# Optimization experiments

Measured on AMD Instinct MI355X. Metric: run time of the kernel, lower is better.

## Reference

```python
import jax, jax.numpy as jnp
import numpy as np


def _topk_corr(h_s, h_t, k):
    """DGMC top-k correspondence: similarity matmul -> top-k -> gather -> dot -> softmax.

    h_s: [B, Ns, C], h_t: [B, Nt, C].
    Mirrors __top_k__ (S_ij = x_s @ x_t^T; topk indices) followed by the
    torch.gather of top-k target embeddings and S_hat = (h_s * h_t[idx]).sum(-1).
    """
    S = jnp.einsum('bsc,btc->bst', h_s, h_t)            # [B, Ns, Nt]
    _, idx = jax.lax.top_k(S, k)                         # [B, Ns, k] (largest sims)
    gathered = jax.vmap(lambda ht, ix: ht[ix])(h_t, idx)  # [B, Ns, k, C]
    S_hat = jnp.einsum('bsc,bskc->bsk', h_s, gathered)    # [B, Ns, k]
    S0 = jax.nn.softmax(S_hat, axis=-1)                   # softmax over k candidates
    return S0, idx


def setup_inputs() -> dict:
    key = jax.random.key(0)
    ks = jax.random.split(key, 4)
    B, Ns, Nt, C = 1, 10000, 10000, 256
    return {
        'eh_s': jax.random.normal(ks[0], (B, Ns, C), jnp.float32),
        'eh_t': jax.random.normal(ks[1], (B, Nt, C), jnp.float32),
        'rh_s': jax.random.normal(ks[2], (B, Ns, C), jnp.float32),
        'rh_t': jax.random.normal(ks[3], (B, Nt, C), jnp.float32),
        'k': 10,
    }


def reference(eh_s, eh_t, rh_s, rh_t, k):
    eS0, eidx = _topk_corr(eh_s, eh_t, k)
    rS0, ridx = _topk_corr(rh_s, rh_t, k)
    # to_sparse via the (all-true, single-graph) dense-batch mask: [B,Ns,k] -> [B*Ns,k]
    B, Ns, kk = eS0.shape
    return eS0.reshape(B * Ns, kk), rS0.reshape(B * Ns, kk), eidx, ridx
```

## Files before the change

kernel.cpp:

```cpp
#include <hip/hip_runtime.h>


typedef __attribute__((ext_vector_type(8)))  short bf16x8;
typedef __attribute__((ext_vector_type(16))) float f32x16;
typedef __attribute__((ext_vector_type(8)))  unsigned short u16x8;

#define K_TOP 10
#define CAND_M 12
#define CDIM 256

#define GLD_LDS(src, dst) \
    __builtin_amdgcn_global_load_lds((const __attribute__((address_space(1))) void*)(src), \
                                     (__attribute__((address_space(3))) void*)(dst), 16, 0, 0)

__device__ __forceinline__ unsigned short f2bf(float f) {
    unsigned u = __float_as_uint(f);
    u += 0x7fffu + ((u >> 16) & 1u);
    return (unsigned short)(u >> 16);
}

__device__ __forceinline__ unsigned umax2(unsigned a, unsigned b) { return a > b ? a : b; }
__device__ __forceinline__ unsigned umax3(unsigned a, unsigned b, unsigned c) {
    return umax2(umax2(a, b), c);
}

__device__ __forceinline__ unsigned umax16(const unsigned (&p)[16]) {
    unsigned x0 = umax3(p[0],  p[1],  p[2]);
    unsigned x1 = umax3(p[3],  p[4],  p[5]);
    unsigned x2 = umax3(p[6],  p[7],  p[8]);
    unsigned x3 = umax3(p[9],  p[10], p[11]);
    unsigned x4 = umax3(p[12], p[13], p[14]);
    return umax2(umax3(x0, x1, x2), umax3(x3, x4, p[15]));
}

template <int K>
__device__ __forceinline__ void sorted_insert(unsigned (&tv)[K], unsigned v) {
    bool m[K];
#pragma unroll
    for (int q = 0; q < K; ++q) m[q] = tv[q] >= v;
    unsigned nv[K];
    nv[0] = m[0] ? tv[0] : v;
#pragma unroll
    for (int q = 1; q < K; ++q)
        nv[q] = m[q] ? tv[q] : (m[q - 1] ? v : tv[q - 1]);
#pragma unroll
    for (int q = 0; q < K; ++q) tv[q] = nv[q];
}

__device__ __forceinline__ void sorted_insert2(unsigned (&tk)[CAND_M], int (&tt)[CAND_M],
                                               unsigned k, int t) {
    bool m[CAND_M];
#pragma unroll
    for (int q = 0; q < CAND_M; ++q) m[q] = tk[q] >= k;
    unsigned nk[CAND_M]; int nt[CAND_M];
    nk[0] = m[0] ? tk[0] : k;
    nt[0] = m[0] ? tt[0] : t;
#pragma unroll
    for (int q = 1; q < CAND_M; ++q) {
        nk[q] = m[q] ? tk[q] : (m[q - 1] ? k : tk[q - 1]);
        nt[q] = m[q] ? tt[q] : (m[q - 1] ? t : tt[q - 1]);
    }
#pragma unroll
    for (int q = 0; q < CAND_M; ++q) { tk[q] = nk[q]; tt[q] = nt[q]; }
}

__global__ void conv_swz2(const float* __restrict__ inE, unsigned short* __restrict__ outE,
                          const float* __restrict__ inR, unsigned short* __restrict__ outR,
                          int N)
{
    int gid = blockIdx.x * blockDim.x + threadIdx.x;
    int half = N * 32;
    const float* in = (gid < half) ? inE : inR;
    unsigned short* out = (gid < half) ? outE : outR;
    int g2 = (gid < half) ? gid : gid - half;
    int row = g2 >> 5, gl = g2 & 31;
    if (row >= N) return;
    const float4* src = (const float4*)(in + (size_t)row * CDIM + gl * 8);
    float4 a0 = src[0], a1 = src[1];
    u16x8 o;
    o[0] = f2bf(a0.x); o[1] = f2bf(a0.y); o[2] = f2bf(a0.z); o[3] = f2bf(a0.w);
    o[4] = f2bf(a1.x); o[5] = f2bf(a1.y); o[6] = f2bf(a1.z); o[7] = f2bf(a1.w);
    *(u16x8*)(out + (size_t)row * CDIM + ((gl ^ (row & 31)) * 8)) = o;
}

__device__ __forceinline__ void stage32(const unsigned short* __restrict__ htb,
                                        short* ldsbuf, int tbase, int Nt,
                                        int tid, int wbase) {
#pragma unroll
    for (int it = 0; it < 4; ++it) {
        int pp = it * 256 + tid;
        int rr = pp >> 5, gg = pp & 31;
        int grow = tbase + rr; grow = grow < Nt ? grow : Nt - 1;
        GLD_LDS(htb + (size_t)grow * CDIM + gg * 8, ldsbuf + (it * 256 + wbase) * 8);
    }
}

__global__ __launch_bounds__(256, 3) void topk_mfma(
    const float* __restrict__ ehs, const float* __restrict__ rhs_,
    const unsigned short* __restrict__ ehtb, const unsigned short* __restrict__ rhtb,
    unsigned* __restrict__ partials, int Ns, int Nt, int Pt, int SB, int PS,
    unsigned VMASK)
{
    __shared__ short ldsT[2 * 32 * 256];

    const int tid = threadIdx.x;
    const int w = tid >> 6, lane = tid & 63;
    const int l5 = lane & 31, hi = lane >> 5;
    const int wbase = tid & ~63;
    const int CH = 2 * Pt;

    const int bid  = blockIdx.x;
    const int prob = bid / (Pt * SB);
    const int rem  = bid % (Pt * SB);
    const int p    = rem / SB, sb = rem % SB;

    const float* hs = prob ? rhs_ : ehs;
    const unsigned short* htb = prob ? rhtb : ehtb;

    const int srow = sb * 128 + w * 32 + l5;
    const int srd  = srow < Ns ? srow : Ns - 1;

    bf16x8 b[16];
#pragma unroll
    for (int kk = 0; kk < 16; ++kk) {
        const float4* sp = (const float4*)(hs + (size_t)srd * CDIM + kk * 16 + hi * 8);
        float4 f0 = sp[0], f1 = sp[1];
        bf16x8 t;
        t[0] = (short)f2bf(f0.x); t[1] = (short)f2bf(f0.y);
        t[2] = (short)f2bf(f0.z); t[3] = (short)f2bf(f0.w);
        t[4] = (short)f2bf(f1.x); t[5] = (short)f2bf(f1.y);
        t[6] = (short)f2bf(f1.z); t[7] = (short)f2bf(f1.w);
        b[kk] = t;
    }

    const int t0 = p * PS;
    const int t1 = min(t0 + PS, Nt);

    unsigned tvp[K_TOP];
#pragma unroll
    for (int q = 0; q < K_TOP; ++q) tvp[q] = 0u;

    const int rounds = (t1 > t0) ? ((t1 - t0 + 31) >> 5) : 0;

    if (rounds > 0) {
        stage32(htb, ldsT, t0, Nt, tid, wbase);
        __syncthreads();

        for (int rd = 0; rd < rounds; ++rd) {
            const int cur = rd & 1;
            const int tb  = t0 + rd * 32;
            if (rd + 1 < rounds)
                stage32(htb, ldsT + (cur ^ 1) * 8192, tb + 32, Nt, tid, wbase);

            const bool guard = (tb + 32 > t1);
            const short* rowp = ldsT + cur * 8192 + l5 * CDIM;
            f32x16 acc;
#pragma unroll
            for (int r = 0; r < 16; ++r) acc[r] = 256.0f;
#pragma unroll
            for (int kk = 0; kk < 16; ++kk) {
                bf16x8 a = *(const bf16x8*)(rowp + (((kk * 2 + hi) ^ l5) * 8));
                acc = __builtin_amdgcn_mfma_f32_32x32x16_bf16(a, b[kk], acc, 0, 0, 0);
            }
            const unsigned ibase = (unsigned)(rd << 4);
            unsigned pu[16];
#pragma unroll
            for (int r = 0; r < 16; ++r)
                pu[r] = (__float_as_uint(acc[r]) & VMASK) | (ibase + (unsigned)r);
            if (guard) {
#pragma unroll
                for (int r = 0; r < 16; ++r) {
                    int t = tb + 4 * hi + (r & 3) + 8 * (r >> 2);
                    if (t >= t1) pu[r] = 0u;
                }
            }
            unsigned mx = umax16(pu);
            while (__any((int)(mx > tvp[K_TOP - 1]))) {
                sorted_insert<K_TOP>(tvp, mx);
#pragma unroll
                for (int r = 0; r < 16; ++r)
                    pu[r] = (pu[r] == mx) ? 0u : pu[r];
                mx = umax16(pu);
            }
            __syncthreads();
        }
    }

    if (srow < Ns) {
        unsigned* wp = partials + ((size_t)(prob * CH + (p * 2 + hi)) * K_TOP) * Ns + srow;
#pragma unroll
        for (int q = 0; q < K_TOP; ++q) wp[(size_t)q * Ns] = tvp[q];
    }
}

__global__ void topk_mergecand(const unsigned* __restrict__ partials, int* __restrict__ cand,
                               int Ns, int CH, int PS, unsigned rdMask)
{
    int g = blockIdx.x * blockDim.x + threadIdx.x;
    if (g >= 2 * Ns) return;
    const int prob = g >= Ns ? 1 : 0;
    const int row  = g - prob * Ns;
    const unsigned* src = partials + ((size_t)prob * CH * K_TOP) * Ns + row;

    unsigned tvk[CAND_M]; int tvt[CAND_M];
#pragma unroll
    for (int q = 0; q < CAND_M; ++q) { tvk[q] = 0u; tvt[q] = 0; }

    for (int c = 0; c < CH; ++c) {
        const int tbase = (c >> 1) * PS + 4 * (c & 1);
#pragma unroll
        for (int q = 0; q < K_TOP; ++q) {
            unsigned k = src[(size_t)(c * K_TOP + q) * Ns];
            if (k > tvk[CAND_M - 1]) {
                unsigned rd = (k >> 4) & rdMask;
                unsigned r  = k & 15u;
                int t = tbase + (int)rd * 32 + (int)((r & 3) + 8 * (r >> 2));
                sorted_insert2(tvk, tvt, k, t);
            }
        }
    }
    int* dst = cand + (size_t)g * CAND_M;
#pragma unroll
    for (int q = 0; q < CAND_M; ++q) dst[q] = tvt[q];
}

__global__ __launch_bounds__(256) void topk_refine(
    const float* __restrict__ ehs, const float* __restrict__ eht,
    const float* __restrict__ rhs_, const float* __restrict__ rht,
    const int* __restrict__ cand, float* __restrict__ out, int Ns)
{
    __shared__ double svd[CAND_M];
    __shared__ int    sci[CAND_M];

    const int wid = blockIdx.x;
    const int tid = threadIdx.x;
    const int m = tid >> 4, c = tid & 15;

    const int prob = wid < Ns ? 0 : 1;
    const int row  = prob ? (wid - Ns) : wid;
    const float* hs = prob ? rhs_ : ehs;
    const float* ht = prob ? rht  : eht;

    if (m < CAND_M) {
        const int t = cand[(size_t)wid * CAND_M + m];
        const float4* ap = (const float4*)(hs + (size_t)row * CDIM);
        const float4* bp = (const float4*)(ht + (size_t)t   * CDIM);

        double s = 0.0;
#pragma unroll
        for (int i = 0; i < 4; ++i) {
            float4 av = ap[c + 16 * i];
            float4 bv = bp[c + 16 * i];
            s += (double)av.x * (double)bv.x + (double)av.y * (double)bv.y
               + (double)av.z * (double)bv.z + (double)av.w * (double)bv.w;
        }
        s += __shfl_xor(s, 1, 64);
        s += __shfl_xor(s, 2, 64);
        s += __shfl_xor(s, 4, 64);
        s += __shfl_xor(s, 8, 64);
        if (c == 0) { svd[m] = s; sci[m] = t; }
    }
    __syncthreads();

    if (tid < 16) {
        const bool act = tid < CAND_M;
        const double sm = act ? svd[tid] : -1.0e300;
        const int    tm = act ? sci[tid] : 0x7FFFFFFF;
        int rank = 0; double vmax = -1.0e300;
#pragma unroll
        for (int j = 0; j < CAND_M; ++j) {
            double vj = svd[j]; int cj = sci[j];
            bool better = (vj > sm) || (vj == sm && cj < tm);
            rank += better ? 1 : 0;
            vmax = fmax(vmax, vj);
        }
        float ex = (act && rank < K_TOP) ? __expf((float)(sm - vmax)) : 0.f;
        float ssum = ex;
        ssum += __shfl_xor(ssum, 1, 64);
        ssum += __shfl_xor(ssum, 2, 64);
        ssum += __shfl_xor(ssum, 4, 64);
        ssum += __shfl_xor(ssum, 8, 64);
        if (act && rank < K_TOP) {
            size_t nsk = (size_t)Ns * K_TOP;
            size_t so  = (size_t)wid * K_TOP;
            out[so + rank] = ex / ssum;
            out[2 * nsk + so + rank] = (float)tm;
        }
    }
}

extern "C" void kernel_launch(void* const* d_in, const int* in_sizes, int n_in,
                              void* d_out, int out_size, void* d_ws, size_t ws_size,
                              hipStream_t stream) {
    (void)n_in; (void)out_size;
    const float* eh_s = (const float*)d_in[0];
    const float* eh_t = (const float*)d_in[1];
    const float* rh_s = (const float*)d_in[2];
    const float* rh_t = (const float*)d_in[3];

    const int Ns = in_sizes[0] / CDIM;
    const int Nt = in_sizes[1] / CDIM;
    const int SB = (Ns + 127) / 128;

    const size_t htbElems = (size_t)Nt * CDIM;
    const size_t htbBytes = 2 * htbElems * 2;
    const size_t candBytes = (size_t)2 * Ns * CAND_M * sizeof(int);

    int Pt = 14;
    while (Pt > 1 &&
           htbBytes + (size_t)2 * Ns * (2 * Pt) * K_TOP * sizeof(unsigned) + candBytes > ws_size)
        Pt -= 1;
    const int PS = (int)((((size_t)Nt + Pt - 1) / Pt + 31) & ~(size_t)31);

    int rdbits = 0;
    while ((1 << rdbits) < (PS >> 5)) ++rdbits;
    const int IDXB = 4 + rdbits;
    const unsigned VMASK  = ~((1u << IDXB) - 1u);
    const unsigned rdMask = (1u << rdbits) - 1u;

    unsigned short* htb_e = (unsigned short*)d_ws;
    unsigned short* htb_r = htb_e + htbElems;
    unsigned* partials = (unsigned*)(htb_r + htbElems);
    int*  cand = (int*)((char*)partials + (size_t)2 * Ns * (2 * Pt) * K_TOP * sizeof(unsigned));

    dim3 block(256);

    int convBlocks = (2 * Nt * 32 + 255) / 256;
    conv_swz2<<<dim3(convBlocks), block, 0, stream>>>(eh_t, htb_e, rh_t, htb_r, Nt);

    topk_mfma<<<dim3(2 * Pt * SB), block, 0, stream>>>(eh_s, rh_s, htb_e, htb_r,
                                                       partials, Ns, Nt, Pt, SB, PS,
                                                       VMASK);

    int nrows = 2 * Ns;
    topk_mergecand<<<dim3((nrows + 255) / 256), block, 0, stream>>>(partials, cand,
                                                                    Ns, 2 * Pt, PS, rdMask);

    topk_refine<<<dim3(nrows), block, 0, stream>>>(eh_s, eh_t, rh_s, rh_t,
                                                   cand, (float*)d_out, Ns);
}
```

Before: 328.0 us.

## Switch similarity MFMA to 16x16x32 tiles with 64 source rows per block

```diff
diff --git a/kernel.cpp b/kernel.cpp
--- a/kernel.cpp
+++ b/kernel.cpp
@@ -2,12 +2,13 @@
 
 
 typedef __attribute__((ext_vector_type(8)))  short bf16x8;
-typedef __attribute__((ext_vector_type(16))) float f32x16;
+typedef __attribute__((ext_vector_type(4)))  float f32x4;
 typedef __attribute__((ext_vector_type(8)))  unsigned short u16x8;
 
 #define K_TOP 10
 #define CAND_M 12
 #define CDIM 256
+#define LDS_HALF 8192
 
 #define GLD_LDS(src, dst) \
     __builtin_amdgcn_global_load_lds((const __attribute__((address_space(1))) void*)(src), \
@@ -24,13 +25,9 @@
     return umax2(umax2(a, b), c);
 }
 
-__device__ __forceinline__ unsigned umax16(const unsigned (&p)[16]) {
-    unsigned x0 = umax3(p[0],  p[1],  p[2]);
-    unsigned x1 = umax3(p[3],  p[4],  p[5]);
-    unsigned x2 = umax3(p[6],  p[7],  p[8]);
-    unsigned x3 = umax3(p[9],  p[10], p[11]);
-    unsigned x4 = umax3(p[12], p[13], p[14]);
-    return umax2(umax3(x0, x1, x2), umax3(x3, x4, p[15]));
+__device__ __forceinline__ unsigned umax8(const unsigned (&p)[8]) {
+    return umax2(umax2(umax3(p[0], p[1], p[2]), umax3(p[3], p[4], p[5])),
+                 umax3(p[6], p[7], p[0]));
 }
 
 template <int K>
@@ -95,19 +92,19 @@
     }
 }
 
-__global__ __launch_bounds__(256, 3) void topk_mfma(
+__global__ __launch_bounds__(256, 4) void topk_mfma(
     const float* __restrict__ ehs, const float* __restrict__ rhs_,
     const unsigned short* __restrict__ ehtb, const unsigned short* __restrict__ rhtb,
     unsigned* __restrict__ partials, int Ns, int Nt, int Pt, int SB, int PS,
     unsigned VMASK)
 {
-    __shared__ short ldsT[2 * 32 * 256];
+    __shared__ short ldsT[2 * LDS_HALF];
 
     const int tid = threadIdx.x;
     const int w = tid >> 6, lane = tid & 63;
-    const int l5 = lane & 31, hi = lane >> 5;
+    const int l4 = lane & 15, q = lane >> 4;
     const int wbase = tid & ~63;
-    const int CH = 2 * Pt;
+    const int CH = 4 * Pt;
 
     const int bid  = blockIdx.x;
     const int prob = bid / (Pt * SB);
@@ -117,13 +114,13 @@
     const float* hs = prob ? rhs_ : ehs;
     const unsigned short* htb = prob ? rhtb : ehtb;
 
-    const int srow = sb * 128 + w * 32 + l5;
+    const int srow = sb * 64 + w * 16 + l4;
     const int srd  = srow < Ns ? srow : Ns - 1;
 
-    bf16x8 b[16];
-#pragma unroll
-    for (int kk = 0; kk < 16; ++kk) {
-        const float4* sp = (const float4*)(hs + (size_t)srd * CDIM + kk * 16 + hi * 8);
+    bf16x8 b[8];
+#pragma unroll
+    for (int kk = 0; kk < 8; ++kk) {
+        const float4* sp = (const float4*)(hs + (size_t)srd * CDIM + kk * 32 + q * 8);
         float4 f0 = sp[0], f1 = sp[1];
         bf16x8 t;
         t[0] = (short)f2bf(f0.x); t[1] = (short)f2bf(f0.y);
@@ -138,7 +135,7 @@
 
     unsigned tvp[K_TOP];
 #pragma unroll
-    for (int q = 0; q < K_TOP; ++q) tvp[q] = 0u;
+    for (int qq = 0; qq < K_TOP; ++qq) tvp[qq] = 0u;
 
     const int rounds = (t1 > t0) ? ((t1 - t0 + 31) >> 5) : 0;
 
@@ -150,46 +147,51 @@
             const int cur = rd & 1;
             const int tb  = t0 + rd * 32;
             if (rd + 1 < rounds)
-                stage32(htb, ldsT + (cur ^ 1) * 8192, tb + 32, Nt, tid, wbase);
+                stage32(htb, ldsT + (cur ^ 1) * LDS_HALF, tb + 32, Nt, tid, wbase);
 
             const bool guard = (tb + 32 > t1);
-            const short* rowp = ldsT + cur * 8192 + l5 * CDIM;
-            f32x16 acc;
-#pragma unroll
-            for (int r = 0; r < 16; ++r) acc[r] = 256.0f;
-#pragma unroll
-            for (int kk = 0; kk < 16; ++kk) {
-                bf16x8 a = *(const bf16x8*)(rowp + (((kk * 2 + hi) ^ l5) * 8));
-                acc = __builtin_amdgcn_mfma_f32_32x32x16_bf16(a, b[kk], acc, 0, 0, 0);
-            }
-            const unsigned ibase = (unsigned)(rd << 4);
-            unsigned pu[16];
-#pragma unroll
-            for (int r = 0; r < 16; ++r)
-                pu[r] = (__float_as_uint(acc[r]) & VMASK) | (ibase + (unsigned)r);
+            const short* base0 = ldsT + cur * LDS_HALF + l4 * CDIM;
+            const short* base1 = base0 + 16 * CDIM;
+            f32x4 acc0, acc1;
+#pragma unroll
+            for (int r = 0; r < 4; ++r) { acc0[r] = 256.0f; acc1[r] = 256.0f; }
+#pragma unroll
+            for (int kk = 0; kk < 8; ++kk) {
+                bf16x8 a0 = *(const bf16x8*)(base0 + (((kk * 4 + q) ^ l4) * 8));
+                acc0 = __builtin_amdgcn_mfma_f32_16x16x32_bf16(a0, b[kk], acc0, 0, 0, 0);
+                bf16x8 a1 = *(const bf16x8*)(base1 + (((kk * 4 + q) ^ (16 + l4)) * 8));
+                acc1 = __builtin_amdgcn_mfma_f32_16x16x32_bf16(a1, b[kk], acc1, 0, 0, 0);
+            }
+            const unsigned ibase = (unsigned)(rd << 3);
+            unsigned pu[8];
+#pragma unroll
+            for (int r = 0; r < 4; ++r) {
+                pu[r]     = (__float_as_uint(acc0[r]) & VMASK) | (ibase + (unsigned)r);
+                pu[4 + r] = (__float_as_uint(acc1[r]) & VMASK) | (ibase + (unsigned)(4 + r));
+            }
             if (guard) {
 #pragma unroll
-                for (int r = 0; r < 16; ++r) {
-                    int t = tb + 4 * hi + (r & 3) + 8 * (r >> 2);
+                for (int r = 0; r < 8; ++r) {
+                    int t = tb + (r & 3) + q * 4 + (r >> 2) * 16;
                     if (t >= t1) pu[r] = 0u;
                 }
             }
-            unsigned mx = umax16(pu);
+            unsigned mx = umax8(pu);
             while (__any((int)(mx > tvp[K_TOP - 1]))) {
                 sorted_insert<K_TOP>(tvp, mx);
 #pragma unroll
-                for (int r = 0; r < 16; ++r)
+                for (int r = 0; r < 8; ++r)
                     pu[r] = (pu[r] == mx) ? 0u : pu[r];
-                mx = umax16(pu);
+                mx = umax8(pu);
             }
             __syncthreads();
         }
     }
 
     if (srow < Ns) {
-        unsigned* wp = partials + ((size_t)(prob * CH + (p * 2 + hi)) * K_TOP) * Ns + srow;
-#pragma unroll
-        for (int q = 0; q < K_TOP; ++q) wp[(size_t)q * Ns] = tvp[q];
+        unsigned* wp = partials + ((size_t)(prob * CH + (p * 4 + q)) * K_TOP) * Ns + srow;
+#pragma unroll
+        for (int qq = 0; qq < K_TOP; ++qq) wp[(size_t)qq * Ns] = tvp[qq];
     }
 }
 
@@ -207,14 +209,14 @@
     for (int q = 0; q < CAND_M; ++q) { tvk[q] = 0u; tvt[q] = 0; }
 
     for (int c = 0; c < CH; ++c) {
-        const int tbase = (c >> 1) * PS + 4 * (c & 1);
+        const int tbase = (c >> 2) * PS + (c & 3) * 4;
 #pragma unroll
         for (int q = 0; q < K_TOP; ++q) {
             unsigned k = src[(size_t)(c * K_TOP + q) * Ns];
             if (k > tvk[CAND_M - 1]) {
-                unsigned rd = (k >> 4) & rdMask;
-                unsigned r  = k & 15u;
-                int t = tbase + (int)rd * 32 + (int)((r & 3) + 8 * (r >> 2));
+                unsigned rd = (k >> 3) & rdMask;
+                unsigned r  = k & 7u;
+                int t = tbase + (int)rd * 32 + (int)((r & 3) + (r >> 2) * 16);
                 sorted_insert2(tvk, tvt, k, t);
             }
         }
@@ -300,7 +302,7 @@
 
     const int Ns = in_sizes[0] / CDIM;
     const int Nt = in_sizes[1] / CDIM;
-    const int SB = (Ns + 127) / 128;
+    const int SB = (Ns + 63) / 64;
 
     const size_t htbElems = (size_t)Nt * CDIM;
     const size_t htbBytes = 2 * htbElems * 2;
@@ -308,20 +310,20 @@
 
     int Pt = 14;
     while (Pt > 1 &&
-           htbBytes + (size_t)2 * Ns * (2 * Pt) * K_TOP * sizeof(unsigned) + candBytes > ws_size)
+           htbBytes + (size_t)2 * Ns * (4 * Pt) * K_TOP * sizeof(unsigned) + candBytes > ws_size)
         Pt -= 1;
     const int PS = (int)((((size_t)Nt + Pt - 1) / Pt + 31) & ~(size_t)31);
 
     int rdbits = 0;
     while ((1 << rdbits) < (PS >> 5)) ++rdbits;
-    const int IDXB = 4 + rdbits;
+    const int IDXB = 3 + rdbits;
     const unsigned VMASK  = ~((1u << IDXB) - 1u);
     const unsigned rdMask = (1u << rdbits) - 1u;
 
     unsigned short* htb_e = (unsigned short*)d_ws;
     unsigned short* htb_r = htb_e + htbElems;
     unsigned* partials = (unsigned*)(htb_r + htbElems);
-    int*  cand = (int*)((char*)partials + (size_t)2 * Ns * (2 * Pt) * K_TOP * sizeof(unsigned));
+    int*  cand = (int*)((char*)partials + (size_t)2 * Ns * (4 * Pt) * K_TOP * sizeof(unsigned));
 
     dim3 block(256);
 
@@ -334,7 +336,7 @@
 
     int nrows = 2 * Ns;
     topk_mergecand<<<dim3((nrows + 255) / 256), block, 0, stream>>>(partials, cand,
-                                                                    Ns, 2 * Pt, PS, rdMask);
+                                                                    Ns, 4 * Pt, PS, rdMask);
 
     topk_refine<<<dim3(nrows), block, 0, stream>>>(eh_s, eh_t, rh_s, rh_t,
                                                    cand, (float*)d_out, Ns);
```

Result: slower. 434.1 us (+32.3%).

## Fuse candidate merge into refine kernel using wave-level max selection

Applied to the files above, without the earlier changes.

```diff
diff --git a/kernel.cpp b/kernel.cpp
--- a/kernel.cpp
+++ b/kernel.cpp
@@ -45,23 +45,6 @@
         nv[q] = m[q] ? tv[q] : (m[q - 1] ? v : tv[q - 1]);
 #pragma unroll
     for (int q = 0; q < K; ++q) tv[q] = nv[q];
-}
-
-__device__ __forceinline__ void sorted_insert2(unsigned (&tk)[CAND_M], int (&tt)[CAND_M],
-                                               unsigned k, int t) {
-    bool m[CAND_M];
-#pragma unroll
-    for (int q = 0; q < CAND_M; ++q) m[q] = tk[q] >= k;
-    unsigned nk[CAND_M]; int nt[CAND_M];
-    nk[0] = m[0] ? tk[0] : k;
-    nt[0] = m[0] ? tt[0] : t;
-#pragma unroll
-    for (int q = 1; q < CAND_M; ++q) {
-        nk[q] = m[q] ? tk[q] : (m[q - 1] ? k : tk[q - 1]);
-        nt[q] = m[q] ? tt[q] : (m[q - 1] ? t : tt[q - 1]);
-    }
-#pragma unroll
-    for (int q = 0; q < CAND_M; ++q) { tk[q] = nk[q]; tt[q] = nt[q]; }
 }
 
 __global__ void conv_swz2(const float* __restrict__ inE, unsigned short* __restrict__ outE,
@@ -193,64 +176,73 @@
     }
 }
 
-__global__ void topk_mergecand(const unsigned* __restrict__ partials, int* __restrict__ cand,
-                               int Ns, int CH, int PS, unsigned rdMask)
-{
-    int g = blockIdx.x * blockDim.x + threadIdx.x;
-    if (g >= 2 * Ns) return;
-    const int prob = g >= Ns ? 1 : 0;
-    const int row  = g - prob * Ns;
-    const unsigned* src = partials + ((size_t)prob * CH * K_TOP) * Ns + row;
-
-    unsigned tvk[CAND_M]; int tvt[CAND_M];
-#pragma unroll
-    for (int q = 0; q < CAND_M; ++q) { tvk[q] = 0u; tvt[q] = 0; }
-
-    for (int c = 0; c < CH; ++c) {
-        const int tbase = (c >> 1) * PS + 4 * (c & 1);
-#pragma unroll
-        for (int q = 0; q < K_TOP; ++q) {
-            unsigned k = src[(size_t)(c * K_TOP + q) * Ns];
-            if (k > tvk[CAND_M - 1]) {
-                unsigned rd = (k >> 4) & rdMask;
-                unsigned r  = k & 15u;
-                int t = tbase + (int)rd * 32 + (int)((r & 3) + 8 * (r >> 2));
-                sorted_insert2(tvk, tvt, k, t);
-            }
-        }
-    }
-    int* dst = cand + (size_t)g * CAND_M;
-#pragma unroll
-    for (int q = 0; q < CAND_M; ++q) dst[q] = tvt[q];
-}
-
 __global__ __launch_bounds__(256) void topk_refine(
     const float* __restrict__ ehs, const float* __restrict__ eht,
     const float* __restrict__ rhs_, const float* __restrict__ rht,
-    const int* __restrict__ cand, float* __restrict__ out, int Ns)
+    const unsigned* __restrict__ partials, float* __restrict__ out,
+    int Ns, int CH, int PS, unsigned rdMask)
 {
     __shared__ double svd[CAND_M];
     __shared__ int    sci[CAND_M];
 
     const int wid = blockIdx.x;
     const int tid = threadIdx.x;
-    const int m = tid >> 4, c = tid & 15;
+    const int m = tid >> 4, c16 = tid & 15;
 
     const int prob = wid < Ns ? 0 : 1;
     const int row  = prob ? (wid - Ns) : wid;
     const float* hs = prob ? rhs_ : ehs;
     const float* ht = prob ? rht  : eht;
 
+    if (tid < CAND_M) sci[tid] = 0;
+
+    if (tid < 64) {
+        const int c = tid;
+        const unsigned* src = partials + ((size_t)prob * CH * K_TOP) * Ns + row;
+        unsigned k0 = 0, k1 = 0, k2 = 0, k3 = 0, k4 = 0,
+                 k5 = 0, k6 = 0, k7 = 0, k8 = 0, k9 = 0;
+        if (c < CH) {
+            const size_t stride = (size_t)Ns;
+            const unsigned* cp = src + (size_t)c * K_TOP * Ns + row - row;
+            cp = src + (size_t)(c * K_TOP) * Ns;
+            k0 = cp[0 * stride]; k1 = cp[1 * stride]; k2 = cp[2 * stride];
+            k3 = cp[3 * stride]; k4 = cp[4 * stride]; k5 = cp[5 * stride];
+            k6 = cp[6 * stride]; k7 = cp[7 * stride]; k8 = cp[8 * stride];
+            k9 = cp[9 * stride];
+        }
+        const int tbase = (c >> 1) * PS + 4 * (c & 1);
+#pragma unroll
+        for (int i = 0; i < CAND_M; ++i) {
+            unsigned mx = k0;
+            mx = umax2(mx, (unsigned)__shfl_xor((int)mx, 1,  64));
+            mx = umax2(mx, (unsigned)__shfl_xor((int)mx, 2,  64));
+            mx = umax2(mx, (unsigned)__shfl_xor((int)mx, 4,  64));
+            mx = umax2(mx, (unsigned)__shfl_xor((int)mx, 8,  64));
+            mx = umax2(mx, (unsigned)__shfl_xor((int)mx, 16, 64));
+            mx = umax2(mx, (unsigned)__shfl_xor((int)mx, 32, 64));
+            unsigned long long ball = __ballot(k0 == mx && c < CH);
+            int owner = (int)__ffsll((unsigned long long)ball) - 1;
+            if (tid == owner) {
+                unsigned rd = (mx >> 4) & rdMask;
+                unsigned r  = mx & 15u;
+                sci[i] = tbase + (int)rd * 32 + (int)((r & 3) + 8 * (r >> 2));
+                k0 = k1; k1 = k2; k2 = k3; k3 = k4; k4 = k5;
+                k5 = k6; k6 = k7; k7 = k8; k8 = k9; k9 = 0u;
+            }
+        }
+    }
+    __syncthreads();
+
     if (m < CAND_M) {
-        const int t = cand[(size_t)wid * CAND_M + m];
+        const int t = sci[m];
         const float4* ap = (const float4*)(hs + (size_t)row * CDIM);
         const float4* bp = (const float4*)(ht + (size_t)t   * CDIM);
 
         double s = 0.0;
 #pragma unroll
         for (int i = 0; i < 4; ++i) {
-            float4 av = ap[c + 16 * i];
-            float4 bv = bp[c + 16 * i];
+            float4 av = ap[c16 + 16 * i];
+            float4 bv = bp[c16 + 16 * i];
             s += (double)av.x * (double)bv.x + (double)av.y * (double)bv.y
                + (double)av.z * (double)bv.z + (double)av.w * (double)bv.w;
         }
@@ -258,7 +250,7 @@
         s += __shfl_xor(s, 2, 64);
         s += __shfl_xor(s, 4, 64);
         s += __shfl_xor(s, 8, 64);
-        if (c == 0) { svd[m] = s; sci[m] = t; }
+        if (c16 == 0) svd[m] = s;
     }
     __syncthreads();
 
@@ -304,11 +296,10 @@
 
     const size_t htbElems = (size_t)Nt * CDIM;
     const size_t htbBytes = 2 * htbElems * 2;
-    const size_t candBytes = (size_t)2 * Ns * CAND_M * sizeof(int);
 
     int Pt = 14;
     while (Pt > 1 &&
-           htbBytes + (size_t)2 * Ns * (2 * Pt) * K_TOP * sizeof(unsigned) + candBytes > ws_size)
+           htbBytes + (size_t)2 * Ns * (2 * Pt) * K_TOP * sizeof(unsigned) > ws_size)
         Pt -= 1;
     const int PS = (int)((((size_t)Nt + Pt - 1) / Pt + 31) & ~(size_t)31);
 
@@ -321,7 +312,6 @@
     unsigned short* htb_e = (unsigned short*)d_ws;
     unsigned short* htb_r = htb_e + htbElems;
     unsigned* partials = (unsigned*)(htb_r + htbElems);
-    int*  cand = (int*)((char*)partials + (size_t)2 * Ns * (2 * Pt) * K_TOP * sizeof(unsigned));
 
     dim3 block(256);
 
@@ -333,9 +323,7 @@
                                                        VMASK);
 
     int nrows = 2 * Ns;
-    topk_mergecand<<<dim3((nrows + 255) / 256), block, 0, stream>>>(partials, cand,
-                                                                    Ns, 2 * Pt, PS, rdMask);
-
     topk_refine<<<dim3(nrows), block, 0, stream>>>(eh_s, eh_t, rh_s, rh_t,
-                                                   cand, (float*)d_out, Ns);
-}
+                                                   partials, (float*)d_out,
+                                                   Ns, 2 * Pt, PS, rdMask);
+}
```

Measured after the change: 279.0 us. -14.9%, faster.
